# Kernel tuning notes

Hardware: AMD Instinct MI355X
Metric: run time of the kernel (lower is better)

## Reference

```python
import jax, jax.numpy as jnp
import numpy as np

B, T, C = 1, 4096, 1024
N_HEAD = 16
HEAD_DIM = C // N_HEAD
SCALE = 1.0 / np.sqrt(HEAD_DIM).astype(np.float32)


def setup_inputs() -> dict:
    key = jax.random.key(0)
    k1, k2, k3 = jax.random.split(key, 3)
    x = jax.random.normal(k1, (B, T, C), dtype=jnp.float32)
    W_attn = jax.random.normal(k2, (C, 3 * C), dtype=jnp.float32) * 0.02
    b_attn = jnp.zeros((3 * C,), dtype=jnp.float32)
    W_proj = jax.random.normal(k3, (C, C), dtype=jnp.float32) * 0.02
    b_proj = jnp.zeros((C,), dtype=jnp.float32)
    return {"x": x, "W_attn": W_attn, "b_attn": b_attn, "W_proj": W_proj, "b_proj": b_proj}


def reference(x, W_attn, b_attn, W_proj, b_proj):
    Bq, Tq, Cq = x.shape
    qkv = x @ W_attn + b_attn                      # [B, T, 3C]
    q, k, v = jnp.split(qkv, 3, axis=-1)
    # split heads -> [B, H, T, D]
    def split_heads(t):
        return t.reshape(Bq, Tq, N_HEAD, HEAD_DIM).transpose(0, 2, 1, 3)
    q, k, v = split_heads(q), split_heads(k), split_heads(v)
    scores = jnp.einsum('bhqd,bhkd->bhqk', q, k) * SCALE  # [B, H, T, T]
    causal = jnp.tril(jnp.ones((Tq, Tq), dtype=bool))
    scores = jnp.where(causal[None, None], scores, jnp.float32(-jnp.inf))
    probs = jax.nn.softmax(scores, axis=-1)
    out = jnp.einsum('bhqk,bhkd->bhqd', probs, v)          # [B, H, T, D]
    out = out.transpose(0, 2, 1, 3).reshape(Bq, Tq, Cq)    # merge heads
    out = out @ W_proj + b_proj
    return out
```

## Files before the change

kernel.cpp:

```cpp
#include <hip/hip_runtime.h>
#include <hip/hip_bf16.h>


typedef unsigned short u16;
typedef u16 u16x4 __attribute__((ext_vector_type(4)));
typedef u16 u16x8 __attribute__((ext_vector_type(8)));
typedef __bf16 bf16x8 __attribute__((ext_vector_type(8)));
typedef float f32x4 __attribute__((ext_vector_type(4)));

#define T_SEQ 4096
#define C_DIM 1024
#define NH 16
#define HD 64
#define QSC 0.18033688f
#define NJOBS 1152

static __device__ __forceinline__ u16 f2bf(float f) {
    __hip_bfloat16 h = __float2bfloat16(f);
    return __builtin_bit_cast(u16, h);
}

static __device__ __forceinline__ float bf2f(u16 u) {
    return __builtin_bit_cast(float, (unsigned)u << 16);
}

static __device__ __forceinline__ bf16x8 ldfr(const u16* base, int byteoff) {
    return __builtin_bit_cast(bf16x8, *(const u16x8*)(base + (byteoff >> 1)));
}

static __device__ __forceinline__ void gld_lds16(const void* g, void* l) {
    __builtin_amdgcn_global_load_lds((const __attribute__((address_space(1))) void*)g,
                                     (__attribute__((address_space(3))) void*)l, 16, 0, 0);
}

#define MFMA16(a, b, c) __builtin_amdgcn_mfma_f32_16x16x32_bf16((a), (b), (c), 0, 0, 0)


__global__ __launch_bounds__(256) void k_prep(const float* __restrict__ x, u16* __restrict__ xb,
                                              const float* __restrict__ W_attn, u16* __restrict__ Wat,
                                              const float* __restrict__ W_proj, u16* __restrict__ Wpt,
                                              unsigned* __restrict__ cnt) {
    const int b = blockIdx.x;
    const int tid = threadIdx.x;
    if (b == 0 && tid == 0) *cnt = 0u;

    if (b < 2048) {
        const int i = (b * 256 + tid) * 8;
        float4 a = *(const float4*)(x + i);
        float4 c = *(const float4*)(x + i + 4);
        u16x8 o;
        o[0] = f2bf(a.x); o[1] = f2bf(a.y); o[2] = f2bf(a.z); o[3] = f2bf(a.w);
        o[4] = f2bf(c.x); o[5] = f2bf(c.y); o[6] = f2bf(c.z); o[7] = f2bf(c.w);
        *(u16x8*)(xb + i) = o;
        return;
    }
    const float* src;
    u16* dst;
    int bx, by, R, Cc;
    if (b < 5120) {
        const int t = b - 2048;
        bx = (t % 96) * 32; by = (t / 96) * 32;
        src = W_attn; dst = Wat; R = 1024; Cc = 3072;
    } else {
        const int t = b - 5120;
        bx = (t & 31) * 32; by = (t >> 5) * 32;
        src = W_proj; dst = Wpt; R = 1024; Cc = 1024;
    }
    __shared__ float tile[32][33];
    const int xi = tid & 31, yi = tid >> 5;
#pragma unroll
    for (int i = 0; i < 32; i += 8)
        tile[yi + i][xi] = src[(size_t)(by + yi + i) * Cc + bx + xi];
    __syncthreads();
#pragma unroll
    for (int i = 0; i < 32; i += 8)
        dst[(size_t)(bx + yi + i) * R + by + xi] = f2bf(tile[xi][yi + i]);
}


template <int EPI>
__global__ __launch_bounds__(256) void k_gemm(const u16* __restrict__ A, const u16* __restrict__ Bt,
                                              const float* __restrict__ bias,
                                              u16* __restrict__ outQ, u16* __restrict__ outK,
                                              u16* __restrict__ outVt, float* __restrict__ outF,
                                              int kd, int nbx) {
    __shared__ u16 Al[128 * 64];
    __shared__ u16 Bl[128 * 64];
    const int tid = threadIdx.x;
    const int lane = tid & 63;
    const int wid = tid >> 6;
    const int wm = wid >> 1, wn = wid & 1;
    const int c = lane & 15, g = lane >> 4;
    const int nwg = gridDim.x;
    const int swzb = ((int)blockIdx.x & 7) * (nwg >> 3) + ((int)blockIdx.x >> 3);
    const int m0 = (swzb % nbx) * 128;
    const int n0 = (swzb / nbx) * 128;
    const int srow = lane >> 3;
    const int sxu = (((lane & 7) * 16) ^ (srow << 4)) >> 1;
    const int swa = (c & 7) << 4;

    f32x4 acc[4][4] = {};

    for (int k0 = 0; k0 < kd; k0 += 64) {
#pragma unroll
        for (int i = 0; i < 4; ++i) {
            const int ch = wid * 4 + i;
            const int row = ch * 8 + srow;
            gld_lds16(A + (size_t)(m0 + row) * kd + k0 + sxu, &Al[ch * 512]);
            gld_lds16(Bt + (size_t)(n0 + row) * kd + k0 + sxu, &Bl[ch * 512]);
        }
        __syncthreads();
        bf16x8 af[4][2], bfm[4][2];
#pragma unroll
        for (int mi = 0; mi < 4; ++mi) {
            const u16* p = Al + (wm * 64 + mi * 16 + c) * 64;
            af[mi][0] = ldfr(p, (16 * g) ^ swa);
            af[mi][1] = ldfr(p, (64 + 16 * g) ^ swa);
        }
#pragma unroll
        for (int ni = 0; ni < 4; ++ni) {
            const u16* p = Bl + (wn * 64 + ni * 16 + c) * 64;
            bfm[ni][0] = ldfr(p, (16 * g) ^ swa);
            bfm[ni][1] = ldfr(p, (64 + 16 * g) ^ swa);
        }
#pragma unroll
        for (int mi = 0; mi < 4; ++mi)
#pragma unroll
            for (int ni = 0; ni < 4; ++ni) {
                acc[mi][ni] = MFMA16(af[mi][0], bfm[ni][0], acc[mi][ni]);
                acc[mi][ni] = MFMA16(af[mi][1], bfm[ni][1], acc[mi][ni]);
            }
        __syncthreads();
    }

    const int mbase = m0 + wm * 64;
    const int nbase = n0 + wn * 64;
    if (EPI == 0) {
        const int part = m0 >> 10;
#pragma unroll
        for (int mi = 0; mi < 4; ++mi) {
            const int fbase = mbase + mi * 16 + 4 * g;
            const f32x4 bv = *(const f32x4*)(bias + fbase);
            const int fr = fbase & 1023;
            const int h = fr >> 6, d0 = fr & 63;
#pragma unroll
            for (int ni = 0; ni < 4; ++ni) {
                const int tok = nbase + ni * 16 + c;
                if (part == 2) {
#pragma unroll
                    for (int r = 0; r < 4; ++r)
                        outVt[(size_t)(fr + r) * T_SEQ + tok] = f2bf(acc[mi][ni][r] + bv[r]);
                } else {
                    u16x4 pk;
#pragma unroll
                    for (int r = 0; r < 4; ++r) {
                        float v = acc[mi][ni][r] + bv[r];
                        pk[r] = f2bf(part == 0 ? v * QSC : v);
                    }
                    u16* dst = (part == 0 ? outQ : outK);
                    *(u16x4*)(dst + (size_t)(h * T_SEQ + tok) * HD + d0) = pk;
                }
            }
        }
    } else {
#pragma unroll
        for (int mi = 0; mi < 4; ++mi) {
            const int fbase = mbase + mi * 16 + 4 * g;
            const f32x4 bv = *(const f32x4*)(bias + fbase);
#pragma unroll
            for (int ni = 0; ni < 4; ++ni) {
                const int tok = nbase + ni * 16 + c;
                f32x4 w;
#pragma unroll
                for (int r = 0; r < 4; ++r) w[r] = acc[mi][ni][r] + bv[r];
                *(f32x4*)(outF + (size_t)tok * C_DIM + fbase) = w;
            }
        }
    }
}


static __device__ __forceinline__ void p_gen(f32x4 s[4], int qabs, int kv0, int g,
                                             bool domask, bf16x8 pa[2]) {
    if (domask) {
#pragma unroll
        for (int tau = 0; tau < 4; ++tau) {
            const int kb = kv0 + 32 * (tau >> 1) + 4 * (tau & 1) + 8 * g;
#pragma unroll
            for (int r = 0; r < 4; ++r)
                if (kb + r > qabs) s[tau][r] = -3e38f;
        }
    }
    u16 pb[4][4];
#pragma unroll
    for (int tau = 0; tau < 4; ++tau)
#pragma unroll
        for (int r = 0; r < 4; ++r)
            pb[tau][r] = f2bf(__builtin_amdgcn_exp2f(s[tau][r]));
    const u16x8 p0 = {pb[0][0], pb[0][1], pb[0][2], pb[0][3], pb[1][0], pb[1][1], pb[1][2], pb[1][3]};
    const u16x8 p1 = {pb[2][0], pb[2][1], pb[2][2], pb[2][3], pb[3][0], pb[3][1], pb[3][2], pb[3][3]};
    pa[0] = __builtin_bit_cast(bf16x8, p0);
    pa[1] = __builtin_bit_cast(bf16x8, p1);
}

__global__ __launch_bounds__(512, 4) void k_flash(const u16* __restrict__ Qg, const u16* __restrict__ Kg,
                                                  const u16* __restrict__ Vtg, u16* __restrict__ Ab,
                                                  u16* __restrict__ part, float* __restrict__ lpart,
                                                  unsigned* __restrict__ cnt) {
    __shared__ u16 sm[4][2][4096];
    __shared__ unsigned jslot;

    const int tid = threadIdx.x;
    const int lane = tid & 63;
    const int wid = tid >> 6;
    const int c = lane & 15, g = lane >> 4;
    const int srow = lane >> 3;
    const int sxu = (((lane & 7) * 16) ^ (srow << 4)) >> 1;

    const u16x8 onespat = {0x3F80, 0x3F80, 0x3F80, 0x3F80, 0x3F80, 0x3F80, 0x3F80, 0x3F80};
    const bf16x8 onesf = __builtin_bit_cast(bf16x8, onespat);

    for (;;) {
        if (tid == 0) jslot = atomicAdd(cnt, 1u);
        __syncthreads();
        const unsigned j = jslot;
        if (j >= (unsigned)NJOBS) break;

        const int head = (int)(j & 15u);
        const int idx = (int)(j >> 4);
        int qb, ch, nc;
        if (idx < 16)      { qb = 15 - (idx >> 3); ch = idx & 7; nc = 8; }
        else if (idx < 30) { const int t = idx - 16; qb = 13 - t / 7;    ch = t % 7; nc = 7; }
        else if (idx < 42) { const int t = idx - 30; qb = 11 - t / 6;    ch = t % 6; nc = 6; }
        else if (idx < 52) { const int t = idx - 42; qb = 9 - t / 5;     ch = t % 5; nc = 5; }
        else if (idx < 60) { const int t = idx - 52; qb = 7 - (t >> 2);  ch = t & 3; nc = 4; }
        else if (idx < 66) { const int t = idx - 60; qb = 5 - t / 3;     ch = t % 3; nc = 3; }
        else if (idx < 70) { const int t = idx - 66; qb = 3 - (t >> 1);  ch = t & 1; nc = 2; }
        else               { qb = 1 - (idx - 70); ch = 0; nc = 1; }
        const int ntile = 4 * qb + 4;
        const int cbase = ntile / nc, crem = ntile % nc;
        const int len = cbase + (ch < crem ? 1 : 0);
        const int start = ch * cbase + (ch < crem ? ch : crem);

        const int q0w = qb * 256 + wid * 32;

        const u16* Qh = Qg + (size_t)head * (T_SEQ * HD);
        const u16* Kh = Kg + (size_t)head * (T_SEQ * HD);
        const u16* Vh = Vtg + (size_t)head * (HD * T_SEQ);

        bf16x8 qf[2][2];
#pragma unroll
        for (int h = 0; h < 2; ++h)
#pragma unroll
            for (int dc = 0; dc < 2; ++dc)
                qf[h][dc] = __builtin_bit_cast(
                    bf16x8, *(const u16x8*)(Qh + (q0w + 16 * h + c) * HD + dc * 32 + 8 * g));

        f32x4 o0[4] = {}, o1[4] = {}, ol0 = {}, ol1 = {};

#pragma unroll
        for (int i = 0; i < 3; ++i) {
            const int ts = (i < len ? start + i : start + len - 1) * 64;
            gld_lds16(Kh + (ts + wid * 8 + srow) * HD + sxu, &sm[i][0][wid * 512]);
            gld_lds16(Vh + (wid * 8 + srow) * T_SEQ + ts + sxu, &sm[i][1][wid * 512]);
        }

        for (int t = 0; t < len; ++t) {
            asm volatile("s_waitcnt vmcnt(4)" ::: "memory");
            __builtin_amdgcn_s_barrier();
            __builtin_amdgcn_sched_barrier(0);
            {
                const int ts = (t + 3 < len ? start + t + 3 : start + len - 1) * 64;
                const int sl = (t + 3) & 3;
                gld_lds16(Kh + (ts + wid * 8 + srow) * HD + sxu, &sm[sl][0][wid * 512]);
                gld_lds16(Vh + (wid * 8 + srow) * T_SEQ + ts + sxu, &sm[sl][1][wid * 512]);
            }
            const int kv0 = (start + t) * 64;
            if (kv0 <= q0w + 31) {
                const u16* Kl = &sm[t & 3][0][0];
                const u16* Vl = &sm[t & 3][1][0];
                f32x4 s0[4], s1[4];
                __builtin_amdgcn_s_setprio(1);
#pragma unroll
                for (int tau = 0; tau < 4; ++tau) {
                    const int prow = 32 * (tau >> 1) + 4 * (tau & 1) + 8 * (c >> 2) + (c & 3);
                    const int sw = (prow & 7) << 4;
                    const u16* kb = Kl + prow * 64;
                    const bf16x8 k0 = ldfr(kb, (16 * g) ^ sw);
                    const bf16x8 k1 = ldfr(kb, (64 + 16 * g) ^ sw);
                    f32x4 z0 = {}, z1 = {};
                    z0 = MFMA16(k0, qf[0][0], z0);
                    s0[tau] = MFMA16(k1, qf[0][1], z0);
                    z1 = MFMA16(k0, qf[1][0], z1);
                    s1[tau] = MFMA16(k1, qf[1][1], z1);
                }
                __builtin_amdgcn_s_setprio(0);
                const bool dm0 = (kv0 + 63) > (q0w);
                const bool dm1 = (kv0 + 63) > (q0w + 16);
                bf16x8 pa0[2], pa1[2];
                p_gen(s0, q0w + c, kv0, g, dm0, pa0);
                p_gen(s1, q0w + 16 + c, kv0, g, dm1, pa1);
                const int swv = (c & 7) << 4;
                __builtin_amdgcn_s_setprio(1);
#pragma unroll
                for (int n = 0; n < 4; ++n) {
                    const u16* vb = Vl + (n * 16 + c) * 64;
                    const bf16x8 v0 = ldfr(vb, (16 * g) ^ swv);
                    const bf16x8 v1 = ldfr(vb, (64 + 16 * g) ^ swv);
                    o0[n] = MFMA16(v0, pa0[0], o0[n]);
                    o0[n] = MFMA16(v1, pa0[1], o0[n]);
                    o1[n] = MFMA16(v0, pa1[0], o1[n]);
                    o1[n] = MFMA16(v1, pa1[1], o1[n]);
                }
                ol0 = MFMA16(onesf, pa0[0], ol0);
                ol0 = MFMA16(onesf, pa0[1], ol0);
                ol1 = MFMA16(onesf, pa1[0], ol1);
                ol1 = MFMA16(onesf, pa1[1], ol1);
                __builtin_amdgcn_s_setprio(0);
            }
        }

        const int ql0 = wid * 32 + c;
        if (nc == 1) {
            const float li0 = 1.0f / ol0[0], li1 = 1.0f / ol1[0];
            u16* dst0 = Ab + (size_t)(qb * 256 + ql0) * C_DIM + head * HD;
            u16* dst1 = dst0 + (size_t)16 * C_DIM;
#pragma unroll
            for (int n = 0; n < 4; ++n) {
                u16x4 w0, w1;
#pragma unroll
                for (int r = 0; r < 4; ++r) {
                    w0[r] = f2bf(o0[n][r] * li0);
                    w1[r] = f2bf(o1[n][r] * li1);
                }
                *(u16x4*)(dst0 + n * 16 + 4 * g) = w0;
                *(u16x4*)(dst1 + n * 16 + 4 * g) = w1;
            }
        } else {
            u16* slot = part + (size_t)j * 16384u;
            float* lsl = lpart + (size_t)j * 256u;
#pragma unroll
            for (int n = 0; n < 4; ++n) {
                u16x4 w0, w1;
#pragma unroll
                for (int r = 0; r < 4; ++r) {
                    w0[r] = f2bf(o0[n][r]);
                    w1[r] = f2bf(o1[n][r]);
                }
                *(u16x4*)(slot + ql0 * 64 + n * 16 + 4 * g) = w0;
                *(u16x4*)(slot + (ql0 + 16) * 64 + n * 16 + 4 * g) = w1;
            }
            if (g == 0) {
                lsl[ql0] = ol0[0];
                lsl[ql0 + 16] = ol1[0];
            }
        }
        __syncthreads();
    }
}


__global__ __launch_bounds__(512) void k_combine(const u16* __restrict__ part,
                                                 const float* __restrict__ lpart,
                                                 u16* __restrict__ Ab) {
    const int head = blockIdx.x / 14;
    const int qb = 2 + (blockIdx.x % 14);
    int nc, idx0;
    if (qb >= 14)      { nc = 8; idx0 = (15 - qb) * 8; }
    else if (qb >= 12) { nc = 7; idx0 = 16 + (13 - qb) * 7; }
    else if (qb >= 10) { nc = 6; idx0 = 30 + (11 - qb) * 6; }
    else if (qb >= 8)  { nc = 5; idx0 = 42 + (9 - qb) * 5; }
    else if (qb >= 6)  { nc = 4; idx0 = 52 + (7 - qb) * 4; }
    else if (qb >= 4)  { nc = 3; idx0 = 60 + (5 - qb) * 3; }
    else               { nc = 2; idx0 = 66 + (3 - qb) * 2; }

    const int q = threadIdx.x >> 1;
    const int dh = (threadIdx.x & 1) * 32;
    float acc[32] = {};
    float l = 0.f;
    for (int i = 0; i < nc; ++i) {
        const unsigned jj = (unsigned)(((idx0 + i) << 4) | head);
        const u16* sp = part + (size_t)jj * 16384u + q * 64 + dh;
#pragma unroll
        for (int v = 0; v < 4; ++v) {
            const u16x8 w = *(const u16x8*)(sp + 8 * v);
#pragma unroll
            for (int e = 0; e < 8; ++e) acc[8 * v + e] += bf2f(w[e]);
        }
        l += lpart[(size_t)jj * 256u + q];
    }
    const float li = 1.0f / l;
    u16* dst = Ab + (size_t)(qb * 256 + q) * C_DIM + head * HD + dh;
#pragma unroll
    for (int v = 0; v < 4; ++v) {
        u16x8 w;
#pragma unroll
        for (int e = 0; e < 8; ++e) w[e] = f2bf(acc[8 * v + e] * li);
        *(u16x8*)(dst + 8 * v) = w;
    }
}


extern "C" void kernel_launch(void* const* d_in, const int* in_sizes, int n_in,
                              void* d_out, int out_size, void* d_ws, size_t ws_size,
                              hipStream_t stream) {
    const float* x      = (const float*)d_in[0];
    const float* W_attn = (const float*)d_in[1];
    const float* b_attn = (const float*)d_in[2];
    const float* W_proj = (const float*)d_in[3];
    const float* b_proj = (const float*)d_in[4];
    float* out = (float*)d_out;

    char* ws = (char*)d_ws;
    u16* xb    = (u16*)(ws);
    u16* Wat   = (u16*)(ws + (8u << 20));
    u16* Wpt   = (u16*)(ws + (14u << 20));
    u16* Qb    = (u16*)(ws + (16u << 20));
    u16* Kb    = (u16*)(ws + (24u << 20));
    u16* Vtb   = (u16*)(ws + (32u << 20));
    u16* prt   = (u16*)(ws + (40u << 20));
    float* lpt = (float*)(ws + (78u << 20));
    u16* Ab    = xb;

    unsigned* cnt = (unsigned*)d_out;

    k_prep<<<6144, 256, 0, stream>>>(x, xb, W_attn, Wat, W_proj, Wpt, cnt);
    k_gemm<0><<<768, 256, 0, stream>>>(Wat, xb, b_attn, Qb, Kb, Vtb, nullptr, 1024, 24);
    k_flash<<<512, 512, 0, stream>>>(Qb, Kb, Vtb, Ab, prt, lpt, cnt);
    k_combine<<<224, 512, 0, stream>>>(prt, lpt, Ab);
    k_gemm<1><<<256, 256, 0, stream>>>(Wpt, Ab, b_proj, nullptr, nullptr, nullptr, out, 1024, 8);
}
```

Baseline: 147.9 us.

## Pipeline GEMM mainloop with 4-stage LDS ring and K-step of 32

Replaces the single-buffered GEMM loop, which had two barriers per K=64 step, with a 4-slot LDS ring buffer of K=32 slices. Three stages are prefetched via direct global-to-LDS loads, and each iteration waits with a partial vmcnt before a single barrier. The LDS layout changes to a fragment-contiguous order with no XOR swizzle, and s_setprio raises wave priority around the MFMA block. The goal is to overlap global loads with MFMA work and drop barrier stalls. The trade-offs are LDS usage rising from 32KB to 64KB, fewer MFMAs per barrier, and a possible rise in LDS bank conflicts from the unswizzled layout.

```diff
diff --git a/kernel.cpp b/kernel.cpp
--- a/kernel.cpp
+++ b/kernel.cpp
@@ -26,6 +26,10 @@
 
 static __device__ __forceinline__ bf16x8 ldfr(const u16* base, int byteoff) {
     return __builtin_bit_cast(bf16x8, *(const u16x8*)(base + (byteoff >> 1)));
+}
+
+static __device__ __forceinline__ bf16x8 ldc(const u16* p) {
+    return __builtin_bit_cast(bf16x8, *(const u16x8*)p);
 }
 
 static __device__ __forceinline__ void gld_lds16(const void* g, void* l) {
@@ -84,8 +88,7 @@
                                               u16* __restrict__ outQ, u16* __restrict__ outK,
                                               u16* __restrict__ outVt, float* __restrict__ outF,
                                               int kd, int nbx) {
-    __shared__ u16 Al[128 * 64];
-    __shared__ u16 Bl[128 * 64];
+    __shared__ u16 sm[4][2][4096];
     const int tid = threadIdx.x;
     const int lane = tid & 63;
     const int wid = tid >> 6;
@@ -95,43 +98,50 @@
     const int swzb = ((int)blockIdx.x & 7) * (nwg >> 3) + ((int)blockIdx.x >> 3);
     const int m0 = (swzb % nbx) * 128;
     const int n0 = (swzb / nbx) * 128;
-    const int srow = lane >> 3;
-    const int sxu = (((lane & 7) * 16) ^ (srow << 4)) >> 1;
-    const int swa = (c & 7) << 4;
+    const int srow = lane & 15;
+    const int scol = (lane >> 4) * 8;
 
     f32x4 acc[4][4] = {};
-
-    for (int k0 = 0; k0 < kd; k0 += 64) {
-#pragma unroll
-        for (int i = 0; i < 4; ++i) {
-            const int ch = wid * 4 + i;
-            const int row = ch * 8 + srow;
-            gld_lds16(A + (size_t)(m0 + row) * kd + k0 + sxu, &Al[ch * 512]);
-            gld_lds16(Bt + (size_t)(n0 + row) * kd + k0 + sxu, &Bl[ch * 512]);
-        }
-        __syncthreads();
-        bf16x8 af[4][2], bfm[4][2];
-#pragma unroll
-        for (int mi = 0; mi < 4; ++mi) {
-            const u16* p = Al + (wm * 64 + mi * 16 + c) * 64;
-            af[mi][0] = ldfr(p, (16 * g) ^ swa);
-            af[mi][1] = ldfr(p, (64 + 16 * g) ^ swa);
-        }
-#pragma unroll
-        for (int ni = 0; ni < 4; ++ni) {
-            const u16* p = Bl + (wn * 64 + ni * 16 + c) * 64;
-            bfm[ni][0] = ldfr(p, (16 * g) ^ swa);
-            bfm[ni][1] = ldfr(p, (64 + 16 * g) ^ swa);
-        }
+    const int nk = kd >> 5;
+
+    auto stage = [&](int s, int sl) {
+        const int k0 = s * 32;
+#pragma unroll
+        for (int i = 0; i < 2; ++i) {
+            const int rb = wid + i * 4;
+            gld_lds16(A + (size_t)(m0 + rb * 16 + srow) * kd + k0 + scol, &sm[sl][0][rb * 512]);
+            gld_lds16(Bt + (size_t)(n0 + rb * 16 + srow) * kd + k0 + scol, &sm[sl][1][rb * 512]);
+        }
+    };
+
+    stage(0, 0);
+    stage(1, 1);
+    stage(2, 2);
+
+    for (int t = 0; t < nk; ++t) {
+        asm volatile("s_waitcnt vmcnt(8)" ::: "memory");
+        __builtin_amdgcn_s_barrier();
+        __builtin_amdgcn_sched_barrier(0);
+        stage(t + 3 < nk ? t + 3 : nk - 1, (t + 3) & 3);
+
+        const u16* Asl = &sm[t & 3][0][0];
+        const u16* Bsl = &sm[t & 3][1][0];
+        bf16x8 af[4], bfm[4];
 #pragma unroll
         for (int mi = 0; mi < 4; ++mi)
-#pragma unroll
-            for (int ni = 0; ni < 4; ++ni) {
-                acc[mi][ni] = MFMA16(af[mi][0], bfm[ni][0], acc[mi][ni]);
-                acc[mi][ni] = MFMA16(af[mi][1], bfm[ni][1], acc[mi][ni]);
-            }
-        __syncthreads();
-    }
+            af[mi] = ldc(Asl + (wm * 4 + mi) * 512 + g * 128 + c * 8);
+#pragma unroll
+        for (int ni = 0; ni < 4; ++ni)
+            bfm[ni] = ldc(Bsl + (wn * 4 + ni) * 512 + g * 128 + c * 8);
+        __builtin_amdgcn_s_setprio(1);
+#pragma unroll
+        for (int mi = 0; mi < 4; ++mi)
+#pragma unroll
+            for (int ni = 0; ni < 4; ++ni)
+                acc[mi][ni] = MFMA16(af[mi], bfm[ni], acc[mi][ni]);
+        __builtin_amdgcn_s_setprio(0);
+    }
+    asm volatile("s_waitcnt vmcnt(0)" ::: "memory");
 
     const int mbase = m0 + wm * 64;
     const int nbase = n0 + wn * 64;
```

Result: slower. 163.7 us (+10.7%).

## Fuse split-KV combine into flash kernel via last-arriver atomic counters

Applied to the files above, without the earlier changes.

Removes the separate combine kernel launch. Each flash block that writes a partial result bumps a per-(head, query-block) completion counter, and the block that arrives last sums all partials, normalizes them and writes the final attention output. This saves one launch and its tail gap, and the combine work overlaps with other flash jobs. In exchange it adds fences, atomics and extra barriers to every partial job, and the counters are zeroed at the start of the output buffer.

```diff
diff --git a/kernel.cpp b/kernel.cpp
--- a/kernel.cpp
+++ b/kernel.cpp
@@ -42,7 +42,9 @@
                                               unsigned* __restrict__ cnt) {
     const int b = blockIdx.x;
     const int tid = threadIdx.x;
-    if (b == 0 && tid == 0) *cnt = 0u;
+    if (b == 0) {
+        for (int i = tid; i < 257; i += 256) cnt[i] = 0u;
+    }
 
     if (b < 2048) {
         const int i = (b * 256 + tid) * 8;
@@ -210,6 +212,8 @@
     __shared__ u16 sm[4][2][4096];
     __shared__ unsigned jslot;
 
+    unsigned* done = cnt + 1;
+
     const int tid = threadIdx.x;
     const int lane = tid & 63;
     const int wid = tid >> 6;
@@ -241,6 +245,7 @@
         const int cbase = ntile / nc, crem = ntile % nc;
         const int len = cbase + (ch < crem ? 1 : 0);
         const int start = ch * cbase + (ch < crem ? ch : crem);
+        const int idx0 = idx - ch;
 
         const int q0w = qb * 256 + wid * 32;
 
@@ -336,6 +341,7 @@
                 *(u16x4*)(dst0 + n * 16 + 4 * g) = w0;
                 *(u16x4*)(dst1 + n * 16 + 4 * g) = w1;
             }
+            __syncthreads();
         } else {
             u16* slot = part + (size_t)j * 16384u;
             float* lsl = lpart + (size_t)j * 256u;
@@ -354,49 +360,41 @@
                 lsl[ql0] = ol0[0];
                 lsl[ql0 + 16] = ol1[0];
             }
-        }
-        __syncthreads();
-    }
-}
-
-
-__global__ __launch_bounds__(512) void k_combine(const u16* __restrict__ part,
-                                                 const float* __restrict__ lpart,
-                                                 u16* __restrict__ Ab) {
-    const int head = blockIdx.x / 14;
-    const int qb = 2 + (blockIdx.x % 14);
-    int nc, idx0;
-    if (qb >= 14)      { nc = 8; idx0 = (15 - qb) * 8; }
-    else if (qb >= 12) { nc = 7; idx0 = 16 + (13 - qb) * 7; }
-    else if (qb >= 10) { nc = 6; idx0 = 30 + (11 - qb) * 6; }
-    else if (qb >= 8)  { nc = 5; idx0 = 42 + (9 - qb) * 5; }
-    else if (qb >= 6)  { nc = 4; idx0 = 52 + (7 - qb) * 4; }
-    else if (qb >= 4)  { nc = 3; idx0 = 60 + (5 - qb) * 3; }
-    else               { nc = 2; idx0 = 66 + (3 - qb) * 2; }
-
-    const int q = threadIdx.x >> 1;
-    const int dh = (threadIdx.x & 1) * 32;
-    float acc[32] = {};
-    float l = 0.f;
-    for (int i = 0; i < nc; ++i) {
-        const unsigned jj = (unsigned)(((idx0 + i) << 4) | head);
-        const u16* sp = part + (size_t)jj * 16384u + q * 64 + dh;
-#pragma unroll
-        for (int v = 0; v < 4; ++v) {
-            const u16x8 w = *(const u16x8*)(sp + 8 * v);
-#pragma unroll
-            for (int e = 0; e < 8; ++e) acc[8 * v + e] += bf2f(w[e]);
-        }
-        l += lpart[(size_t)jj * 256u + q];
-    }
-    const float li = 1.0f / l;
-    u16* dst = Ab + (size_t)(qb * 256 + q) * C_DIM + head * HD + dh;
-#pragma unroll
-    for (int v = 0; v < 4; ++v) {
-        u16x8 w;
-#pragma unroll
-        for (int e = 0; e < 8; ++e) w[e] = f2bf(acc[8 * v + e] * li);
-        *(u16x8*)(dst + 8 * v) = w;
+            __threadfence();
+            __syncthreads();
+            if (tid == 0)
+                jslot = __hip_atomic_fetch_add(&done[head * 16 + qb], 1u,
+                                               __ATOMIC_ACQ_REL, __HIP_MEMORY_SCOPE_AGENT);
+            __syncthreads();
+            if (jslot == (unsigned)(nc - 1)) {
+                __threadfence();
+                const int q = tid >> 1;
+                const int dh = (tid & 1) * 32;
+                float av[32] = {};
+                float lsum = 0.f;
+                for (int i = 0; i < nc; ++i) {
+                    const unsigned jj = (unsigned)(((idx0 + i) << 4) | head);
+                    const u16* sp = part + (size_t)jj * 16384u + q * 64 + dh;
+#pragma unroll
+                    for (int v = 0; v < 4; ++v) {
+                        const u16x8 w = *(const u16x8*)(sp + 8 * v);
+#pragma unroll
+                        for (int e = 0; e < 8; ++e) av[8 * v + e] += bf2f(w[e]);
+                    }
+                    lsum += lpart[(size_t)jj * 256u + q];
+                }
+                const float li = 1.0f / lsum;
+                u16* dst = Ab + (size_t)(qb * 256 + q) * C_DIM + head * HD + dh;
+#pragma unroll
+                for (int v = 0; v < 4; ++v) {
+                    u16x8 w;
+#pragma unroll
+                    for (int e = 0; e < 8; ++e) w[e] = f2bf(av[8 * v + e] * li);
+                    *(u16x8*)(dst + 8 * v) = w;
+                }
+            }
+            __syncthreads();
+        }
     }
 }
 
@@ -427,6 +425,5 @@
     k_prep<<<6144, 256, 0, stream>>>(x, xb, W_attn, Wat, W_proj, Wpt, cnt);
     k_gemm<0><<<768, 256, 0, stream>>>(Wat, xb, b_attn, Qb, Kb, Vtb, nullptr, 1024, 24);
     k_flash<<<512, 512, 0, stream>>>(Qb, Kb, Vtb, Ab, prt, lpt, cnt);
-    k_combine<<<224, 512, 0, stream>>>(prt, lpt, Ab);
     k_gemm<1><<<256, 256, 0, stream>>>(Wpt, Ab, b_proj, nullptr, nullptr, nullptr, out, 1024, 8);
 }
```

Result: slower. 541.9 us (+266.4%).
